# Kernel optimization log

Measured on AMD Instinct MI355X. Metric: run time of the kernel, lower is better.

The kernel has to match this reference:

```python
import jax, jax.numpy as jnp
import numpy as np

N = 100000   # nodes
E = 1600000  # edges
DIM = 64
DIMS = [128, 64, 64, 64]  # [2*DIM] + 3*[DIM]
MAX_DEG = 64
NUM_LAB = 16

def _leaky(x):
    return jnp.where(x >= 0, x, 0.01 * x)

def _bn(x, g, b, eps=1e-5):
    # BatchNorm1d in training mode: per-feature batch mean / biased variance
    m = x.mean(axis=0)
    v = x.var(axis=0)
    return (x - m) * jax.lax.rsqrt(v + eps) * g + b

def setup_inputs() -> dict:
    key = jax.random.key(0)
    ks = jax.random.split(key, 40)
    d = {}
    d["node_deg"] = jax.random.randint(ks[0], (N,), 0, MAX_DEG + 1)
    d["node_lab"] = jax.random.randint(ks[1], (N,), 0, NUM_LAB)
    d["edge_index"] = jax.random.randint(ks[2], (2, E), 0, N)
    d["emb_deg"] = jax.random.normal(ks[3], (MAX_DEG + 1, DIM), jnp.float32) * 0.1
    d["emb_lab"] = jax.random.normal(ks[4], (NUM_LAB, DIM), jnp.float32) * 0.1
    k = 5
    for i, (n1, n2) in enumerate(zip(DIMS[:-1], DIMS[1:])):
        d[f"w{i}"] = jax.random.normal(ks[k], (n2, n1), jnp.float32) / np.sqrt(n1); k += 1
        d[f"b{i}"] = jnp.zeros((n2,), jnp.float32)
        d[f"g{i}"] = jnp.ones((n2,), jnp.float32)
        d[f"be{i}"] = jnp.zeros((n2,), jnp.float32)
    SUMD = sum(DIMS)  # 320
    d["fw1"] = jax.random.normal(ks[k], (DIM, SUMD), jnp.float32) / np.sqrt(SUMD); k += 1
    d["fb1"] = jnp.zeros((DIM,), jnp.float32)
    d["fg"] = jnp.ones((DIM,), jnp.float32)
    d["fbe"] = jnp.zeros((DIM,), jnp.float32)
    d["fw2"] = jax.random.normal(ks[k], (1, DIM), jnp.float32) / np.sqrt(DIM)
    d["fb2"] = jnp.zeros((1,), jnp.float32)
    return d

def reference(node_deg, node_lab, edge_index, emb_deg, emb_lab,
              w0, b0, g0, be0, w1, b1, g1, be1, w2, b2, g2, be2,
              fw1, fb1, fg, fbe, fw2, fb2):
    src, dst = edge_index[0], edge_index[1]
    # input embedding: concat of degree and label embeddings -> [N, 128]
    x0 = jnp.concatenate([emb_deg[node_deg], emb_lab[node_lab]], axis=1)
    z = [x0]
    for (w, b, g, be) in [(w0, b0, g0, be0), (w1, b1, g1, be1), (w2, b2, g2, be2)]:
        x = z[-1]
        # GINConv (eps=0): h = Linear(x + sum_{j in N(i)} x_j)
        agg = jax.ops.segment_sum(x[src], dst, num_segments=N)
        h = (x + agg) @ w.T + b
        z.append(_leaky(_bn(h, g, be)))
    xc = jnp.concatenate(z, axis=1)  # [N, 320]
    h = _leaky(_bn(xc @ fw1.T + fb1, fg, fbe))
    return jax.nn.sigmoid(h @ fw2.T + fb2).squeeze()  # [N]
```

## Files before the change

### kernel.cpp

```cpp
#include <hip/hip_runtime.h>
#include <math.h>

typedef __bf16 bf16;
typedef __attribute__((ext_vector_type(8))) __bf16 bf16x8;
typedef __attribute__((ext_vector_type(4))) float f32x4;

#define NBLK 128
#define NB_MAX 1600

__device__ __forceinline__ void bn_coeffs(const float* st, const float* g,
                                          const float* be, float inv_n, int d,
                                          float& sc, float& sh) {
  float mean = st[d] * inv_n;
  float var = st[64 + d] * inv_n - mean * mean;
  sc = g[d] * rsqrtf(var + 1e-5f);
  sh = be[d] - mean * sc;
}

__global__ __launch_bounds__(256) void bin_hist_kernel(const int* __restrict__ dst,
                                                       int* __restrict__ cnt,
                                                       int E, int ch, int nb) {
  __shared__ int lcnt[NB_MAX];
  int tid = threadIdx.x, blk = blockIdx.x;
  for (int t = tid; t < nb; t += 256) lcnt[t] = 0;
  __syncthreads();
  int base = blk * ch, eend = min(E, base + ch);
  for (int e = base + tid; e < eend; e += 256) atomicAdd(&lcnt[dst[e] >> 6], 1);
  __syncthreads();
  for (int t = tid; t < nb; t += 256) cnt[blk * nb + t] = lcnt[t];
}

__global__ __launch_bounds__(256) void bin_meta_kernel(const int* __restrict__ cnt,
                                                       int* __restrict__ bucketptr,
                                                       int* __restrict__ woff, int nb) {
  __shared__ int stot[NB_MAX];
  __shared__ int lds[256];
  int tid = threadIdx.x;
  for (int i = tid; i < nb; i += 256) {
    int s = 0;
    for (int blk = 0; blk < NBLK; ++blk) s += cnt[blk * nb + i];
    stot[i] = s;
  }
  __syncthreads();
  const int CH = 7;
  int vals[CH];
  int s = 0;
#pragma unroll
  for (int k = 0; k < CH; ++k) {
    int i = tid * CH + k;
    vals[k] = (i < nb) ? stot[i] : 0;
    s += vals[k];
  }
  lds[tid] = s;
  __syncthreads();
  for (int off = 1; off < 256; off <<= 1) {
    int v = (tid >= off) ? lds[tid - off] : 0;
    __syncthreads();
    lds[tid] += v;
    __syncthreads();
  }
  int run = lds[tid] - s;
  if (tid == 0) bucketptr[0] = 0;
#pragma unroll
  for (int k = 0; k < CH; ++k) {
    int i = tid * CH + k;
    int ex = run;
    run += vals[k];
    if (i < nb) { bucketptr[i + 1] = run; stot[i] = ex; }
  }
  __syncthreads();
  for (int i = tid; i < nb; i += 256) {
    int run2 = stot[i];
    for (int blk = 0; blk < NBLK; ++blk) {
      woff[blk * nb + i] = run2;
      run2 += cnt[blk * nb + i];
    }
  }
}

__global__ __launch_bounds__(256) void bin_scatter_kernel(const int* __restrict__ src,
                                                          const int* __restrict__ dst,
                                                          const int* __restrict__ woff,
                                                          int* __restrict__ packed,
                                                          int E, int ch, int nb) {
  __shared__ int cur[NB_MAX];
  int tid = threadIdx.x, blk = blockIdx.x;
  for (int t = tid; t < nb; t += 256) cur[t] = woff[blk * nb + t];
  __syncthreads();
  int base = blk * ch, eend = min(E, base + ch);
  for (int e = base + tid; e < eend; e += 256) {
    int d = dst[e], s = src[e];
    int pos = atomicAdd(&cur[d >> 6], 1);
    packed[pos] = ((d & 63) << 17) | s;
  }
}

__global__ __launch_bounds__(256) void csr_finalize_kernel(
    const int* __restrict__ packed, const int* __restrict__ bucketptr,
    int* __restrict__ rowptr, int* __restrict__ colidx, int n, int E) {
  __shared__ int hist[64], offs[64];
  int tid = threadIdx.x, b = blockIdx.x;
  if (tid < 64) hist[tid] = 0;
  __syncthreads();
  int beg = bucketptr[b], end = bucketptr[b + 1];
  for (int e = beg + tid; e < end; e += 256) atomicAdd(&hist[packed[e] >> 17], 1);
  __syncthreads();
  if (tid == 0) {
    int run = 0;
    for (int j = 0; j < 64; ++j) { offs[j] = run; run += hist[j]; }
  }
  __syncthreads();
  if (tid < 64) {
    int idx = b * 64 + tid;
    if (idx < n) rowptr[idx] = beg + offs[tid];
    hist[tid] = offs[tid];
  }
  if (b == 0 && tid == 64) rowptr[n] = E;
  __syncthreads();
  for (int e = beg + tid; e < end; e += 256) {
    int w = packed[e];
    int pos = atomicAdd(&hist[w >> 17], 1);
    colidx[beg + pos] = w & 0x1FFFF;
  }
}

__global__ __launch_bounds__(256) void mfma_gemm0(
    const int* __restrict__ deg, const int* __restrict__ lab,
    const float* __restrict__ ed, const float* __restrict__ el,
    const float* __restrict__ W, bf16* __restrict__ x0,
    bf16* __restrict__ y, int n) {
  __shared__ bf16 As[64][136];
  __shared__ bf16 Bs[64][136];
  int tid = threadIdx.x;
  int nbase = blockIdx.x * 64;
  {
    int r = tid >> 2, c = tid & 3;
    int node = nbase + r;
    union { bf16 hh[32]; uint4 u[4]; } t;
    if (node < n) {
      int idx = (c < 2) ? deg[node] : lab[node];
      const float* srcp = (c < 2) ? (ed + (size_t)idx * 64 + c * 32)
                                  : (el + (size_t)idx * 64 + (c - 2) * 32);
#pragma unroll
      for (int j = 0; j < 8; ++j) {
        float4 f = ((const float4*)srcp)[j];
        t.hh[j * 4 + 0] = (bf16)f.x; t.hh[j * 4 + 1] = (bf16)f.y;
        t.hh[j * 4 + 2] = (bf16)f.z; t.hh[j * 4 + 3] = (bf16)f.w;
      }
#pragma unroll
      for (int j = 0; j < 4; ++j)
        *(uint4*)(x0 + (size_t)node * 128 + c * 32 + j * 8) = t.u[j];
    } else {
#pragma unroll
      for (int j = 0; j < 4; ++j) t.u[j] = uint4{0, 0, 0, 0};
    }
#pragma unroll
    for (int j = 0; j < 4; ++j) *(uint4*)&As[r][c * 32 + j * 8] = t.u[j];
    const float4* wp = (const float4*)(W + r * 128 + c * 32);
#pragma unroll
    for (int j = 0; j < 4; ++j) {
      float4 f0 = wp[j * 2], f1 = wp[j * 2 + 1];
      union { bf16 h[8]; uint4 u; } tw;
      tw.h[0] = (bf16)f0.x; tw.h[1] = (bf16)f0.y; tw.h[2] = (bf16)f0.z; tw.h[3] = (bf16)f0.w;
      tw.h[4] = (bf16)f1.x; tw.h[5] = (bf16)f1.y; tw.h[6] = (bf16)f1.z; tw.h[7] = (bf16)f1.w;
      *(uint4*)&Bs[r][c * 32 + j * 8] = tw.u;
    }
  }
  __syncthreads();
  int l = tid & 63, w = tid >> 6, m = l & 15, quad = l >> 4;
  f32x4 acc[4] = {{0.f, 0.f, 0.f, 0.f}, {0.f, 0.f, 0.f, 0.f},
                  {0.f, 0.f, 0.f, 0.f}, {0.f, 0.f, 0.f, 0.f}};
#pragma unroll
  for (int k0 = 0; k0 < 128; k0 += 32) {
    bf16x8 a = *(const bf16x8*)&As[w * 16 + m][k0 + quad * 8];
#pragma unroll
    for (int t = 0; t < 4; ++t) {
      bf16x8 b = *(const bf16x8*)&Bs[t * 16 + m][k0 + quad * 8];
      acc[t] = __builtin_amdgcn_mfma_f32_16x16x32_bf16(a, b, acc[t], 0, 0, 0);
    }
  }
#pragma unroll
  for (int t = 0; t < 4; ++t)
#pragma unroll
    for (int r4 = 0; r4 < 4; ++r4) {
      int node = nbase + w * 16 + quad * 4 + r4;
      if (node < n) y[(size_t)node * 64 + t * 16 + m] = (bf16)acc[t][r4];
    }
}

__global__ __launch_bounds__(256) void mfma_gemm_bn(
    const bf16* __restrict__ hin, const float* __restrict__ st,
    const float* __restrict__ g, const float* __restrict__ be, float inv_n,
    const float* __restrict__ W, bf16* __restrict__ z,
    bf16* __restrict__ y, int n) {
  __shared__ bf16 As[64][72];
  __shared__ bf16 Bs[64][72];
  __shared__ float ssc[64], ssh[64];
  int tid = threadIdx.x;
  int nbase = blockIdx.x * 64;
  if (tid < 64) {
    float sc, sh;
    bn_coeffs(st, g, be, inv_n, tid, sc, sh);
    ssc[tid] = sc; ssh[tid] = sh;
  }
  __syncthreads();
  {
    int r = tid >> 2, c = tid & 3;
    int node = nbase + r;
    union { bf16 h[16]; uint4 u[2]; } t;
    if (node < n) {
      const uint4* p = (const uint4*)(hin + (size_t)node * 64 + c * 16);
      union { uint4 u; bf16 h[8]; } a0, a1;
      a0.u = p[0]; a1.u = p[1];
#pragma unroll
      for (int j = 0; j < 8; ++j) {
        int d = c * 16 + j;
        float v = (float)a0.h[j] * ssc[d] + ssh[d];
        v = (v >= 0.f) ? v : 0.01f * v;
        t.h[j] = (bf16)v;
      }
#pragma unroll
      for (int j = 0; j < 8; ++j) {
        int d = c * 16 + 8 + j;
        float v = (float)a1.h[j] * ssc[d] + ssh[d];
        v = (v >= 0.f) ? v : 0.01f * v;
        t.h[8 + j] = (bf16)v;
      }
      *(uint4*)(z + (size_t)node * 64 + c * 16) = t.u[0];
      *(uint4*)(z + (size_t)node * 64 + c * 16 + 8) = t.u[1];
    } else {
      t.u[0] = uint4{0, 0, 0, 0}; t.u[1] = uint4{0, 0, 0, 0};
    }
    *(uint4*)&As[r][c * 16] = t.u[0];
    *(uint4*)&As[r][c * 16 + 8] = t.u[1];
    const float4* wp = (const float4*)(W + r * 64 + c * 16);
#pragma unroll
    for (int j = 0; j < 2; ++j) {
      float4 f0 = wp[j * 2], f1 = wp[j * 2 + 1];
      union { bf16 h[8]; uint4 u; } tw;
      tw.h[0] = (bf16)f0.x; tw.h[1] = (bf16)f0.y; tw.h[2] = (bf16)f0.z; tw.h[3] = (bf16)f0.w;
      tw.h[4] = (bf16)f1.x; tw.h[5] = (bf16)f1.y; tw.h[6] = (bf16)f1.z; tw.h[7] = (bf16)f1.w;
      *(uint4*)&Bs[r][c * 16 + j * 8] = tw.u;
    }
  }
  __syncthreads();
  int l = tid & 63, w = tid >> 6, m = l & 15, quad = l >> 4;
  f32x4 acc[4] = {{0.f, 0.f, 0.f, 0.f}, {0.f, 0.f, 0.f, 0.f},
                  {0.f, 0.f, 0.f, 0.f}, {0.f, 0.f, 0.f, 0.f}};
#pragma unroll
  for (int k0 = 0; k0 < 64; k0 += 32) {
    bf16x8 a = *(const bf16x8*)&As[w * 16 + m][k0 + quad * 8];
#pragma unroll
    for (int t = 0; t < 4; ++t) {
      bf16x8 b = *(const bf16x8*)&Bs[t * 16 + m][k0 + quad * 8];
      acc[t] = __builtin_amdgcn_mfma_f32_16x16x32_bf16(a, b, acc[t], 0, 0, 0);
    }
  }
#pragma unroll
  for (int t = 0; t < 4; ++t)
#pragma unroll
    for (int r4 = 0; r4 < 4; ++r4) {
      int node = nbase + w * 16 + quad * 4 + r4;
      if (node < n) y[(size_t)node * 64 + t * 16 + m] = (bf16)acc[t][r4];
    }
}

__global__ __launch_bounds__(256) void gather_kernel(
    const bf16* __restrict__ y, const int* __restrict__ rowptr,
    const int* __restrict__ colidx, const float* __restrict__ bias,
    bf16* __restrict__ h, float* __restrict__ stats, int n) {
  __shared__ float s_sum[64], s_sq[64];
  int tid = threadIdx.x;
  if (tid < 64) { s_sum[tid] = 0.f; s_sq[tid] = 0.f; }
  __syncthreads();
  int lane = tid & 63, wv = tid >> 6;
  int half = lane >> 5;
  int lh = lane & 31;
  const unsigned* y32 = (const unsigned*)y;
  unsigned* h32 = (unsigned*)h;
  float b0 = bias[2 * lh], b1 = bias[2 * lh + 1];
  float p0 = 0, p1 = 0, q0 = 0, q1 = 0;
  int stride = gridDim.x * 8;
  for (int nodeA = blockIdx.x * 8 + wv * 2; nodeA < n; nodeA += stride) {
    int nodeB = nodeA + 1;
    bool hasB = nodeB < n;
    float a0 = 0, a1 = 0, c0 = 0, c1 = 0;
    int e0 = rowptr[nodeA], f0 = rowptr[nodeA + 1];
    int e1 = hasB ? rowptr[nodeB] : 0;
    int f1 = hasB ? rowptr[nodeB + 1] : 0;
    while (e0 + 8 <= f0 && e1 + 8 <= f1) {
#pragma unroll
      for (int k = 0; k < 4; ++k) {
        int sA = colidx[e0 + 2 * k + half];
        int sB = colidx[e1 + 2 * k + half];
        unsigned dA = y32[(size_t)sA * 32 + lh];
        unsigned dB = y32[(size_t)sB * 32 + lh];
        union { unsigned u; float f; } t0, t1, t2, t3;
        t0.u = dA << 16; t1.u = dA & 0xFFFF0000u;
        t2.u = dB << 16; t3.u = dB & 0xFFFF0000u;
        a0 += t0.f; a1 += t1.f; c0 += t2.f; c1 += t3.f;
      }
      e0 += 8; e1 += 8;
    }
    for (; e0 + 8 <= f0; e0 += 8) {
#pragma unroll
      for (int k = 0; k < 4; ++k) {
        int s = colidx[e0 + 2 * k + half];
        unsigned d = y32[(size_t)s * 32 + lh];
        union { unsigned u; float f; } t0, t1;
        t0.u = d << 16; t1.u = d & 0xFFFF0000u;
        a0 += t0.f; a1 += t1.f;
      }
    }
    for (; e0 + 2 <= f0; e0 += 2) {
      int s = colidx[e0 + half];
      unsigned d = y32[(size_t)s * 32 + lh];
      union { unsigned u; float f; } t0, t1;
      t0.u = d << 16; t1.u = d & 0xFFFF0000u;
      a0 += t0.f; a1 += t1.f;
    }
    if (e0 < f0) {
      int s = colidx[e0];
      unsigned d = y32[(size_t)s * 32 + lh];
      if (half == 0) {
        union { unsigned u; float f; } t0, t1;
        t0.u = d << 16; t1.u = d & 0xFFFF0000u;
        a0 += t0.f; a1 += t1.f;
      }
    }
    for (; e1 + 8 <= f1; e1 += 8) {
#pragma unroll
      for (int k = 0; k < 4; ++k) {
        int s = colidx[e1 + 2 * k + half];
        unsigned d = y32[(size_t)s * 32 + lh];
        union { unsigned u; float f; } t0, t1;
        t0.u = d << 16; t1.u = d & 0xFFFF0000u;
        c0 += t0.f; c1 += t1.f;
      }
    }
    for (; e1 + 2 <= f1; e1 += 2) {
      int s = colidx[e1 + half];
      unsigned d = y32[(size_t)s * 32 + lh];
      union { unsigned u; float f; } t0, t1;
      t0.u = d << 16; t1.u = d & 0xFFFF0000u;
      c0 += t0.f; c1 += t1.f;
    }
    if (e1 < f1) {
      int s = colidx[e1];
      unsigned d = y32[(size_t)s * 32 + lh];
      if (half == 0) {
        union { unsigned u; float f; } t0, t1;
        t0.u = d << 16; t1.u = d & 0xFFFF0000u;
        c0 += t0.f; c1 += t1.f;
      }
    }
    a0 += __shfl_xor(a0, 32); a1 += __shfl_xor(a1, 32);
    c0 += __shfl_xor(c0, 32); c1 += __shfl_xor(c1, 32);
    int node = half ? nodeB : nodeA;
    float u0 = half ? c0 : a0;
    float u1 = half ? c1 : a1;
    if (half == 0 || hasB) {
      unsigned sd = y32[(size_t)node * 32 + lh];
      union { unsigned u; float f; } s0, s1;
      s0.u = sd << 16; s1.u = sd & 0xFFFF0000u;
      float v0 = u0 + s0.f + b0;
      float v1 = u1 + s1.f + b1;
      union { bf16 hh[2]; unsigned u; } o;
      o.hh[0] = (bf16)v0; o.hh[1] = (bf16)v1;
      h32[(size_t)node * 32 + lh] = o.u;
      p0 += v0; q0 += v0 * v0;
      p1 += v1; q1 += v1 * v1;
    }
  }
  atomicAdd(&s_sum[2 * lh], p0); atomicAdd(&s_sq[2 * lh], q0);
  atomicAdd(&s_sum[2 * lh + 1], p1); atomicAdd(&s_sq[2 * lh + 1], q1);
  __syncthreads();
  if (tid < 64) {
    atomicAdd(&stats[tid], s_sum[tid]);
    atomicAdd(&stats[64 + tid], s_sq[tid]);
  }
}

__global__ __launch_bounds__(256) void mfma_final(
    const bf16* __restrict__ x0, const bf16* __restrict__ z1,
    const bf16* __restrict__ z2, const bf16* __restrict__ h2,
    const float* __restrict__ st2, const float* __restrict__ g2,
    const float* __restrict__ be2, float inv_n,
    const float* __restrict__ fw1, const float* __restrict__ fb1,
    bf16* __restrict__ hf, float* __restrict__ stats, int n) {
  __shared__ bf16 As[64][136];
  __shared__ bf16 Bs[64][136];
  __shared__ float s_sum[64], s_sq[64], ssc[64], ssh[64];
  int tid = threadIdx.x;
  if (tid < 64) {
    s_sum[tid] = 0.f; s_sq[tid] = 0.f;
    float sc, sh;
    bn_coeffs(st2, g2, be2, inv_n, tid, sc, sh);
    ssc[tid] = sc; ssh[tid] = sh;
  }
  int nbase = blockIdx.x * 64;
  int l = tid & 63, w = tid >> 6, m = l & 15, quad = l >> 4;
  int r = tid >> 2, c = tid & 3;
  int node_r = nbase + r;
  f32x4 acc[4] = {{0.f, 0.f, 0.f, 0.f}, {0.f, 0.f, 0.f, 0.f},
                  {0.f, 0.f, 0.f, 0.f}, {0.f, 0.f, 0.f, 0.f}};

#pragma unroll
  for (int seg = 0; seg < 4; ++seg) {
    __syncthreads();
    if (seg == 0) {
      uint4 v[4] = {};
      if (node_r < n) {
        const uint4* p = (const uint4*)(x0 + (size_t)node_r * 128 + c * 32);
#pragma unroll
        for (int j = 0; j < 4; ++j) v[j] = p[j];
      }
#pragma unroll
      for (int j = 0; j < 4; ++j) *(uint4*)&As[r][c * 32 + j * 8] = v[j];
      const float4* wp = (const float4*)(fw1 + r * 320 + c * 32);
#pragma unroll
      for (int j = 0; j < 4; ++j) {
        float4 f0 = wp[j * 2], f1 = wp[j * 2 + 1];
        union { bf16 h[8]; uint4 u; } t;
        t.h[0] = (bf16)f0.x; t.h[1] = (bf16)f0.y; t.h[2] = (bf16)f0.z; t.h[3] = (bf16)f0.w;
        t.h[4] = (bf16)f1.x; t.h[5] = (bf16)f1.y; t.h[6] = (bf16)f1.z; t.h[7] = (bf16)f1.w;
        *(uint4*)&Bs[r][c * 32 + j * 8] = t.u;
      }
    } else if (seg < 3) {
      const bf16* zz = (seg == 1) ? z1 : z2;
      uint4 v[2] = {};
      if (node_r < n) {
        const uint4* p = (const uint4*)(zz + (size_t)node_r * 64 + c * 16);
        v[0] = p[0]; v[1] = p[1];
      }
      *(uint4*)&As[r][c * 16] = v[0];
      *(uint4*)&As[r][c * 16 + 8] = v[1];
      const float4* wp = (const float4*)(fw1 + r * 320 + (seg == 1 ? 128 : 192) + c * 16);
#pragma unroll
      for (int j = 0; j < 2; ++j) {
        float4 f0 = wp[j * 2], f1 = wp[j * 2 + 1];
        union { bf16 h[8]; uint4 u; } t;
        t.h[0] = (bf16)f0.x; t.h[1] = (bf16)f0.y; t.h[2] = (bf16)f0.z; t.h[3] = (bf16)f0.w;
        t.h[4] = (bf16)f1.x; t.h[5] = (bf16)f1.y; t.h[6] = (bf16)f1.z; t.h[7] = (bf16)f1.w;
        *(uint4*)&Bs[r][c * 16 + j * 8] = t.u;
      }
    } else {
      union { bf16 h[16]; uint4 u[2]; } t;
      if (node_r < n) {
        const uint4* p = (const uint4*)(h2 + (size_t)node_r * 64 + c * 16);
        union { uint4 u; bf16 h[8]; } a0, a1;
        a0.u = p[0]; a1.u = p[1];
#pragma unroll
        for (int j = 0; j < 8; ++j) {
          int d = c * 16 + j;
          float v = (float)a0.h[j] * ssc[d] + ssh[d];
          v = (v >= 0.f) ? v : 0.01f * v;
          t.h[j] = (bf16)v;
        }
#pragma unroll
        for (int j = 0; j < 8; ++j) {
          int d = c * 16 + 8 + j;
          float v = (float)a1.h[j] * ssc[d] + ssh[d];
          v = (v >= 0.f) ? v : 0.01f * v;
          t.h[8 + j] = (bf16)v;
        }
      } else {
        t.u[0] = uint4{0, 0, 0, 0}; t.u[1] = uint4{0, 0, 0, 0};
      }
      *(uint4*)&As[r][c * 16] = t.u[0];
      *(uint4*)&As[r][c * 16 + 8] = t.u[1];
      const float4* wp = (const float4*)(fw1 + r * 320 + 256 + c * 16);
#pragma unroll
      for (int j = 0; j < 2; ++j) {
        float4 f0 = wp[j * 2], f1 = wp[j * 2 + 1];
        union { bf16 h[8]; uint4 u; } tw;
        tw.h[0] = (bf16)f0.x; tw.h[1] = (bf16)f0.y; tw.h[2] = (bf16)f0.z; tw.h[3] = (bf16)f0.w;
        tw.h[4] = (bf16)f1.x; tw.h[5] = (bf16)f1.y; tw.h[6] = (bf16)f1.z; tw.h[7] = (bf16)f1.w;
        *(uint4*)&Bs[r][c * 16 + j * 8] = tw.u;
      }
    }
    __syncthreads();
    int kmax = (seg == 0) ? 128 : 64;
    for (int k0 = 0; k0 < kmax; k0 += 32) {
      bf16x8 a = *(const bf16x8*)&As[w * 16 + m][k0 + quad * 8];
#pragma unroll
      for (int t = 0; t < 4; ++t) {
        bf16x8 b = *(const bf16x8*)&Bs[t * 16 + m][k0 + quad * 8];
        acc[t] = __builtin_amdgcn_mfma_f32_16x16x32_bf16(a, b, acc[t], 0, 0, 0);
      }
    }
  }

#pragma unroll
  for (int t = 0; t < 4; ++t) {
    int o = t * 16 + m;
    float bv = fb1[o];
    float s = 0.f, q = 0.f;
#pragma unroll
    for (int r4 = 0; r4 < 4; ++r4) {
      int node = nbase + w * 16 + quad * 4 + r4;
      if (node < n) {
        float v = acc[t][r4] + bv;
        hf[(size_t)node * 64 + o] = (bf16)v;
        s += v;
        q += v * v;
      }
    }
    atomicAdd(&s_sum[o], s);
    atomicAdd(&s_sq[o], q);
  }
  __syncthreads();
  if (tid < 64) {
    atomicAdd(&stats[tid], s_sum[tid]);
    atomicAdd(&stats[64 + tid], s_sq[tid]);
  }
}

__global__ __launch_bounds__(256) void final_out_kernel(
    const bf16* __restrict__ hf, const float* __restrict__ st,
    const float* __restrict__ g, const float* __restrict__ be, float inv_n,
    const float* __restrict__ fw2, const float* __restrict__ fb2,
    float* __restrict__ out, int n) {
  int lane = threadIdx.x & 63;
  int node = blockIdx.x * 4 + (threadIdx.x >> 6);
  if (node >= n) return;
  float sc, sh;
  bn_coeffs(st, g, be, inv_n, lane, sc, sh);
  float v = (float)hf[(size_t)node * 64 + lane] * sc + sh;
  v = (v >= 0.f) ? v : 0.01f * v;
  v *= fw2[lane];
#pragma unroll
  for (int off = 32; off > 0; off >>= 1) v += __shfl_xor(v, off);
  if (lane == 0) out[node] = 1.f / (1.f + expf(-(v + fb2[0])));
}

extern "C" void kernel_launch(void* const* d_in, const int* in_sizes, int n_in,
                              void* d_out, int out_size, void* d_ws, size_t ws_size,
                              hipStream_t stream) {
  const int* node_deg = (const int*)d_in[0];
  const int* node_lab = (const int*)d_in[1];
  const int* ei = (const int*)d_in[2];
  const float* emb_deg = (const float*)d_in[3];
  const float* emb_lab = (const float*)d_in[4];
  const float* w0 = (const float*)d_in[5];
  const float* b0 = (const float*)d_in[6];
  const float* g0 = (const float*)d_in[7];
  const float* be0 = (const float*)d_in[8];
  const float* w1 = (const float*)d_in[9];
  const float* b1 = (const float*)d_in[10];
  const float* g1 = (const float*)d_in[11];
  const float* be1 = (const float*)d_in[12];
  const float* w2 = (const float*)d_in[13];
  const float* b2 = (const float*)d_in[14];
  const float* g2 = (const float*)d_in[15];
  const float* be2 = (const float*)d_in[16];
  const float* fw1 = (const float*)d_in[17];
  const float* fb1 = (const float*)d_in[18];
  const float* fg = (const float*)d_in[19];
  const float* fbe = (const float*)d_in[20];
  const float* fw2 = (const float*)d_in[21];
  const float* fb2 = (const float*)d_in[22];

  const int N = in_sizes[0];
  const int E = in_sizes[2] / 2;
  const int* src = ei;
  const int* dst = ei + E;
  const int NB = (N + 63) >> 6;
  const int CH = (E + NBLK - 1) / NBLK;
  const float inv_n = 1.0f / N;

  char* ws = (char*)d_ws;
  size_t off = 0;
  auto alloc = [&](size_t bytes) {
    void* p = ws + off;
    off += (bytes + 255) & ~(size_t)255;
    return p;
  };
  bf16* x0 = (bf16*)alloc((size_t)N * 128 * 2);
  bf16* z1 = (bf16*)alloc((size_t)N * 64 * 2);
  bf16* z2 = (bf16*)alloc((size_t)N * 64 * 2);
  bf16* h = (bf16*)alloc((size_t)N * 64 * 2);
  bf16* y = (bf16*)alloc((size_t)N * 64 * 2);
  int* packed = (int*)alloc((size_t)E * 4);
  int* colidx = (int*)alloc((size_t)E * 4);
  int* rowptr = (int*)alloc((size_t)(N + 1) * 4);
  int* cnt = (int*)alloc((size_t)NBLK * NB * 4);
  int* woff = (int*)alloc((size_t)NBLK * NB * 4);
  int* bucketptr = (int*)alloc((size_t)(NB + 1) * 4);
  float* stats = (float*)alloc(4 * 256 * 4);

  hipMemsetAsync(stats, 0, 4 * 256 * 4, stream);

  bin_hist_kernel<<<NBLK, 256, 0, stream>>>(dst, cnt, E, CH, NB);
  bin_meta_kernel<<<1, 256, 0, stream>>>(cnt, bucketptr, woff, NB);
  bin_scatter_kernel<<<NBLK, 256, 0, stream>>>(src, dst, woff, packed, E, CH, NB);
  csr_finalize_kernel<<<NB, 256, 0, stream>>>(packed, bucketptr, rowptr, colidx, N, E);

  int ngrid = (N + 63) / 64;
  int ggrid = 2048;

  mfma_gemm0<<<ngrid, 256, 0, stream>>>(node_deg, node_lab, emb_deg, emb_lab, w0, x0, y, N);
  gather_kernel<<<ggrid, 256, 0, stream>>>(y, rowptr, colidx, b0, h, stats, N);
  mfma_gemm_bn<<<ngrid, 256, 0, stream>>>(h, stats, g0, be0, inv_n, w1, z1, y, N);
  gather_kernel<<<ggrid, 256, 0, stream>>>(y, rowptr, colidx, b1, h, stats + 256, N);
  mfma_gemm_bn<<<ngrid, 256, 0, stream>>>(h, stats + 256, g1, be1, inv_n, w2, z2, y, N);
  gather_kernel<<<ggrid, 256, 0, stream>>>(y, rowptr, colidx, b2, h, stats + 512, N);
  mfma_final<<<ngrid, 256, 0, stream>>>(x0, z1, z2, h, stats + 512, g2, be2, inv_n,
                                        fw1, fb1, y, stats + 768, N);
  final_out_kernel<<<(N + 3) / 4, 256, 0, stream>>>(y, stats + 768, fg, fbe, inv_n,
                                                    fw2, fb2, (float*)d_out, N);
}
```

Measured before the change: 596.0 us.

## Split bucket metadata into parallel kernels and gather four nodes per wave

The single-block bucket metadata kernel becomes three kernels: a multi-block column sum, a single-block scan, and a multi-block write-offset pass. This spreads the serial 128-way loops over more compute units. The gather kernel now processes four nodes per wave instead of two, interleaving two dual-node steps so more independent loads are in flight. The cost is two extra kernel launches and higher register pressure in the gather loop.

Measured after the change: 572.2 us. 4.0% less time.

```diff
diff --git a/kernel.cpp b/kernel.cpp
--- a/kernel.cpp
+++ b/kernel.cpp
@@ -30,25 +30,26 @@
   for (int t = tid; t < nb; t += 256) cnt[blk * nb + t] = lcnt[t];
 }
 
-__global__ __launch_bounds__(256) void bin_meta_kernel(const int* __restrict__ cnt,
-                                                       int* __restrict__ bucketptr,
-                                                       int* __restrict__ woff, int nb) {
-  __shared__ int stot[NB_MAX];
+__global__ __launch_bounds__(256) void bin_tot_kernel(const int* __restrict__ cnt,
+                                                      int* __restrict__ tot, int nb) {
+  int b = blockIdx.x * 256 + threadIdx.x;
+  if (b >= nb) return;
+  int s = 0;
+  for (int blk = 0; blk < NBLK; ++blk) s += cnt[blk * nb + b];
+  tot[b] = s;
+}
+
+__global__ __launch_bounds__(256) void scan_buckets_kernel(const int* __restrict__ tot,
+                                                           int* __restrict__ bucketptr, int nb) {
   __shared__ int lds[256];
   int tid = threadIdx.x;
-  for (int i = tid; i < nb; i += 256) {
-    int s = 0;
-    for (int blk = 0; blk < NBLK; ++blk) s += cnt[blk * nb + i];
-    stot[i] = s;
-  }
-  __syncthreads();
   const int CH = 7;
   int vals[CH];
   int s = 0;
 #pragma unroll
   for (int k = 0; k < CH; ++k) {
     int i = tid * CH + k;
-    vals[k] = (i < nb) ? stot[i] : 0;
+    vals[k] = (i < nb) ? tot[i] : 0;
     s += vals[k];
   }
   lds[tid] = s;
@@ -64,17 +65,20 @@
 #pragma unroll
   for (int k = 0; k < CH; ++k) {
     int i = tid * CH + k;
-    int ex = run;
     run += vals[k];
-    if (i < nb) { bucketptr[i + 1] = run; stot[i] = ex; }
-  }
-  __syncthreads();
-  for (int i = tid; i < nb; i += 256) {
-    int run2 = stot[i];
-    for (int blk = 0; blk < NBLK; ++blk) {
-      woff[blk * nb + i] = run2;
-      run2 += cnt[blk * nb + i];
-    }
+    if (i < nb) bucketptr[i + 1] = run;
+  }
+}
+
+__global__ __launch_bounds__(256) void bin_off_kernel(const int* __restrict__ cnt,
+                                                      const int* __restrict__ bucketptr,
+                                                      int* __restrict__ woff, int nb) {
+  int b = blockIdx.x * 256 + threadIdx.x;
+  if (b >= nb) return;
+  int run = bucketptr[b];
+  for (int blk = 0; blk < NBLK; ++blk) {
+    woff[blk * nb + b] = run;
+    run += cnt[blk * nb + b];
   }
 }
 
@@ -265,6 +269,55 @@
     }
 }
 
+__device__ __forceinline__ void dual_step(const unsigned* __restrict__ y32,
+                                          const int* __restrict__ colidx,
+                                          int e0, int e1, int half, int lh,
+                                          float& a0, float& a1, float& c0, float& c1) {
+#pragma unroll
+  for (int k = 0; k < 4; ++k) {
+    int sA = colidx[e0 + 2 * k + half];
+    int sB = colidx[e1 + 2 * k + half];
+    unsigned dA = y32[(size_t)sA * 32 + lh];
+    unsigned dB = y32[(size_t)sB * 32 + lh];
+    union { unsigned u; float f; } t0, t1, t2, t3;
+    t0.u = dA << 16; t1.u = dA & 0xFFFF0000u;
+    t2.u = dB << 16; t3.u = dB & 0xFFFF0000u;
+    a0 += t0.f; a1 += t1.f; c0 += t2.f; c1 += t3.f;
+  }
+}
+
+__device__ __forceinline__ void solo_accum(const unsigned* __restrict__ y32,
+                                           const int* __restrict__ colidx,
+                                           int& e, int f, int half, int lh,
+                                           float& a0, float& a1) {
+  for (; e + 8 <= f; e += 8) {
+#pragma unroll
+    for (int k = 0; k < 4; ++k) {
+      int s = colidx[e + 2 * k + half];
+      unsigned d = y32[(size_t)s * 32 + lh];
+      union { unsigned u; float f; } t0, t1;
+      t0.u = d << 16; t1.u = d & 0xFFFF0000u;
+      a0 += t0.f; a1 += t1.f;
+    }
+  }
+  for (; e + 2 <= f; e += 2) {
+    int s = colidx[e + half];
+    unsigned d = y32[(size_t)s * 32 + lh];
+    union { unsigned u; float f; } t0, t1;
+    t0.u = d << 16; t1.u = d & 0xFFFF0000u;
+    a0 += t0.f; a1 += t1.f;
+  }
+  if (e < f) {
+    int s = colidx[e];
+    unsigned d = y32[(size_t)s * 32 + lh];
+    if (half == 0) {
+      union { unsigned u; float f; } t0, t1;
+      t0.u = d << 16; t1.u = d & 0xFFFF0000u;
+      a0 += t0.f; a1 += t1.f;
+    }
+  }
+}
+
 __global__ __launch_bounds__(256) void gather_kernel(
     const bf16* __restrict__ y, const int* __restrict__ rowptr,
     const int* __restrict__ colidx, const float* __restrict__ bias,
@@ -280,96 +333,69 @@
   unsigned* h32 = (unsigned*)h;
   float b0 = bias[2 * lh], b1 = bias[2 * lh + 1];
   float p0 = 0, p1 = 0, q0 = 0, q1 = 0;
-  int stride = gridDim.x * 8;
-  for (int nodeA = blockIdx.x * 8 + wv * 2; nodeA < n; nodeA += stride) {
-    int nodeB = nodeA + 1;
-    bool hasB = nodeB < n;
-    float a0 = 0, a1 = 0, c0 = 0, c1 = 0;
-    int e0 = rowptr[nodeA], f0 = rowptr[nodeA + 1];
-    int e1 = hasB ? rowptr[nodeB] : 0;
-    int f1 = hasB ? rowptr[nodeB + 1] : 0;
-    while (e0 + 8 <= f0 && e1 + 8 <= f1) {
-#pragma unroll
-      for (int k = 0; k < 4; ++k) {
-        int sA = colidx[e0 + 2 * k + half];
-        int sB = colidx[e1 + 2 * k + half];
-        unsigned dA = y32[(size_t)sA * 32 + lh];
-        unsigned dB = y32[(size_t)sB * 32 + lh];
-        union { unsigned u; float f; } t0, t1, t2, t3;
-        t0.u = dA << 16; t1.u = dA & 0xFFFF0000u;
-        t2.u = dB << 16; t3.u = dB & 0xFFFF0000u;
-        a0 += t0.f; a1 += t1.f; c0 += t2.f; c1 += t3.f;
-      }
-      e0 += 8; e1 += 8;
-    }
-    for (; e0 + 8 <= f0; e0 += 8) {
-#pragma unroll
-      for (int k = 0; k < 4; ++k) {
-        int s = colidx[e0 + 2 * k + half];
-        unsigned d = y32[(size_t)s * 32 + lh];
-        union { unsigned u; float f; } t0, t1;
-        t0.u = d << 16; t1.u = d & 0xFFFF0000u;
-        a0 += t0.f; a1 += t1.f;
-      }
-    }
-    for (; e0 + 2 <= f0; e0 += 2) {
-      int s = colidx[e0 + half];
-      unsigned d = y32[(size_t)s * 32 + lh];
-      union { unsigned u; float f; } t0, t1;
-      t0.u = d << 16; t1.u = d & 0xFFFF0000u;
-      a0 += t0.f; a1 += t1.f;
-    }
-    if (e0 < f0) {
-      int s = colidx[e0];
-      unsigned d = y32[(size_t)s * 32 + lh];
-      if (half == 0) {
-        union { unsigned u; float f; } t0, t1;
-        t0.u = d << 16; t1.u = d & 0xFFFF0000u;
-        a0 += t0.f; a1 += t1.f;
-      }
-    }
-    for (; e1 + 8 <= f1; e1 += 8) {
-#pragma unroll
-      for (int k = 0; k < 4; ++k) {
-        int s = colidx[e1 + 2 * k + half];
-        unsigned d = y32[(size_t)s * 32 + lh];
-        union { unsigned u; float f; } t0, t1;
-        t0.u = d << 16; t1.u = d & 0xFFFF0000u;
-        c0 += t0.f; c1 += t1.f;
-      }
-    }
-    for (; e1 + 2 <= f1; e1 += 2) {
-      int s = colidx[e1 + half];
-      unsigned d = y32[(size_t)s * 32 + lh];
-      union { unsigned u; float f; } t0, t1;
-      t0.u = d << 16; t1.u = d & 0xFFFF0000u;
-      c0 += t0.f; c1 += t1.f;
-    }
-    if (e1 < f1) {
-      int s = colidx[e1];
-      unsigned d = y32[(size_t)s * 32 + lh];
-      if (half == 0) {
-        union { unsigned u; float f; } t0, t1;
-        t0.u = d << 16; t1.u = d & 0xFFFF0000u;
-        c0 += t0.f; c1 += t1.f;
-      }
-    }
+  int stride = gridDim.x * 16;
+  for (int n0 = blockIdx.x * 16 + wv * 4; n0 < n; n0 += stride) {
+    int n1 = n0 + 1, n2 = n0 + 2, n3 = n0 + 3;
+    bool h1 = n1 < n, h2 = n2 < n, h3 = n3 < n;
+    float a0 = 0, a1 = 0, b0v = 0, b1v = 0, c0 = 0, c1 = 0, d0 = 0, d1 = 0;
+    int eA0 = rowptr[n0], fA0 = rowptr[n0 + 1];
+    int eA1 = h1 ? rowptr[n1] : 0, fA1 = h1 ? rowptr[n1 + 1] : 0;
+    int eB0 = h2 ? rowptr[n2] : 0, fB0 = h2 ? rowptr[n2 + 1] : 0;
+    int eB1 = h3 ? rowptr[n3] : 0, fB1 = h3 ? rowptr[n3 + 1] : 0;
+    while (eA0 + 8 <= fA0 && eA1 + 8 <= fA1 && eB0 + 8 <= fB0 && eB1 + 8 <= fB1) {
+      dual_step(y32, colidx, eA0, eA1, half, lh, a0, a1, b0v, b1v);
+      dual_step(y32, colidx, eB0, eB1, half, lh, c0, c1, d0, d1);
+      eA0 += 8; eA1 += 8; eB0 += 8; eB1 += 8;
+    }
+    while (eA0 + 8 <= fA0 && eA1 + 8 <= fA1) {
+      dual_step(y32, colidx, eA0, eA1, half, lh, a0, a1, b0v, b1v);
+      eA0 += 8; eA1 += 8;
+    }
+    while (eB0 + 8 <= fB0 && eB1 + 8 <= fB1) {
+      dual_step(y32, colidx, eB0, eB1, half, lh, c0, c1, d0, d1);
+      eB0 += 8; eB1 += 8;
+    }
+    solo_accum(y32, colidx, eA0, fA0, half, lh, a0, a1);
+    solo_accum(y32, colidx, eA1, fA1, half, lh, b0v, b1v);
+    solo_accum(y32, colidx, eB0, fB0, half, lh, c0, c1);
+    solo_accum(y32, colidx, eB1, fB1, half, lh, d0, d1);
     a0 += __shfl_xor(a0, 32); a1 += __shfl_xor(a1, 32);
+    b0v += __shfl_xor(b0v, 32); b1v += __shfl_xor(b1v, 32);
     c0 += __shfl_xor(c0, 32); c1 += __shfl_xor(c1, 32);
-    int node = half ? nodeB : nodeA;
-    float u0 = half ? c0 : a0;
-    float u1 = half ? c1 : a1;
-    if (half == 0 || hasB) {
-      unsigned sd = y32[(size_t)node * 32 + lh];
-      union { unsigned u; float f; } s0, s1;
-      s0.u = sd << 16; s1.u = sd & 0xFFFF0000u;
-      float v0 = u0 + s0.f + b0;
-      float v1 = u1 + s1.f + b1;
-      union { bf16 hh[2]; unsigned u; } o;
-      o.hh[0] = (bf16)v0; o.hh[1] = (bf16)v1;
-      h32[(size_t)node * 32 + lh] = o.u;
-      p0 += v0; q0 += v0 * v0;
-      p1 += v1; q1 += v1 * v1;
+    d0 += __shfl_xor(d0, 32); d1 += __shfl_xor(d1, 32);
+    {
+      int node = half ? n1 : n0;
+      float u0 = half ? b0v : a0;
+      float u1 = half ? b1v : a1;
+      if (half == 0 || h1) {
+        unsigned sd = y32[(size_t)node * 32 + lh];
+        union { unsigned u; float f; } s0, s1;
+        s0.u = sd << 16; s1.u = sd & 0xFFFF0000u;
+        float v0 = u0 + s0.f + b0;
+        float v1 = u1 + s1.f + b1;
+        union { bf16 hh[2]; unsigned u; } o;
+        o.hh[0] = (bf16)v0; o.hh[1] = (bf16)v1;
+        h32[(size_t)node * 32 + lh] = o.u;
+        p0 += v0; q0 += v0 * v0;
+        p1 += v1; q1 += v1 * v1;
+      }
+    }
+    {
+      int node = half ? n3 : n2;
+      float u0 = half ? d0 : c0;
+      float u1 = half ? d1 : c1;
+      if ((half == 0 && h2) || (half == 1 && h3)) {
+        unsigned sd = y32[(size_t)node * 32 + lh];
+        union { unsigned u; float f; } s0, s1;
+        s0.u = sd << 16; s1.u = sd & 0xFFFF0000u;
+        float v0 = u0 + s0.f + b0;
+        float v1 = u1 + s1.f + b1;
+        union { bf16 hh[2]; unsigned u; } o;
+        o.hh[0] = (bf16)v0; o.hh[1] = (bf16)v1;
+        h32[(size_t)node * 32 + lh] = o.u;
+        p0 += v0; q0 += v0 * v0;
+        p1 += v1; q1 += v1 * v1;
+      }
     }
   }
   atomicAdd(&s_sum[2 * lh], p0); atomicAdd(&s_sq[2 * lh], q0);
@@ -586,13 +612,16 @@
   int* rowptr = (int*)alloc((size_t)(N + 1) * 4);
   int* cnt = (int*)alloc((size_t)NBLK * NB * 4);
   int* woff = (int*)alloc((size_t)NBLK * NB * 4);
+  int* btot = (int*)alloc((size_t)NB * 4);
   int* bucketptr = (int*)alloc((size_t)(NB + 1) * 4);
   float* stats = (float*)alloc(4 * 256 * 4);
 
   hipMemsetAsync(stats, 0, 4 * 256 * 4, stream);
 
   bin_hist_kernel<<<NBLK, 256, 0, stream>>>(dst, cnt, E, CH, NB);
-  bin_meta_kernel<<<1, 256, 0, stream>>>(cnt, bucketptr, woff, NB);
+  bin_tot_kernel<<<(NB + 255) / 256, 256, 0, stream>>>(cnt, btot, NB);
+  scan_buckets_kernel<<<1, 256, 0, stream>>>(btot, bucketptr, NB);
+  bin_off_kernel<<<(NB + 255) / 256, 256, 0, stream>>>(cnt, bucketptr, woff, NB);
   bin_scatter_kernel<<<NBLK, 256, 0, stream>>>(src, dst, woff, packed, E, CH, NB);
   csr_finalize_kernel<<<NB, 256, 0, stream>>>(packed, bucketptr, rowptr, colidx, N, E);
 
```
